# Performance work log

Measured on AMD Instinct MI355X. Metric: run time of the kernel, lower is better.

The kernel has to match this reference:

```python
import jax, jax.numpy as jnp
import numpy as np

B, SEQ, EMB, HID = 256, 256, 128, 512
NG = 1          # n_glimpses
CEXP = 10.0     # tanh_exploration
NEG = -1e9      # masked-logit value (stands in for -inf)


def setup_inputs():
    key = jax.random.key(0)
    ks = jax.random.split(key, 19)
    se = 1.0 / np.sqrt(EMB)
    sh = 1.0 / np.sqrt(HID)
    u = lambda k, shape, s: jax.random.uniform(k, shape, jnp.float32, -s, s)
    return {
        'embedding': u(ks[0], (SEQ, EMB), 1.0),
        'enc_Wih': u(ks[1], (4 * HID, EMB), sh),
        'enc_Whh': u(ks[2], (4 * HID, HID), sh),
        'enc_b': u(ks[3], (4 * HID,), sh),
        'dec_Wih': u(ks[4], (4 * HID, EMB), sh),
        'dec_Whh': u(ks[5], (4 * HID, HID), sh),
        'dec_b': u(ks[6], (4 * HID,), sh),
        'pt_Wq': u(ks[7], (HID, HID), sh), 'pt_bq': u(ks[8], (HID,), sh),
        'pt_Wref': u(ks[9], (HID, HID), sh), 'pt_bref': u(ks[10], (HID,), sh),
        'pt_V': u(ks[11], (HID,), sh),
        'gl_Wq': u(ks[12], (HID, HID), sh), 'gl_bq': u(ks[13], (HID,), sh),
        'gl_Wref': u(ks[14], (HID, HID), sh), 'gl_bref': u(ks[15], (HID,), sh),
        'gl_V': u(ks[16], (HID,), sh),
        'dec_start': u(ks[17], (EMB,), se),
        'inputs': jax.random.randint(ks[18], (B, SEQ), 0, SEQ),
    }


def lstm_cell(x, h, c, Wih, Whh, b):
    # PyTorch gate order: i, f, g, o
    g = x @ Wih.T + h @ Whh.T + b
    i, f, gg, o = jnp.split(g, 4, axis=1)
    c = jax.nn.sigmoid(f) * c + jax.nn.sigmoid(i) * jnp.tanh(gg)
    h = jax.nn.sigmoid(o) * jnp.tanh(c)
    return h, c


def reference(embedding, enc_Wih, enc_Whh, enc_b,
              dec_Wih, dec_Whh, dec_b,
              pt_Wq, pt_bq, pt_Wref, pt_bref, pt_V,
              gl_Wq, gl_bq, gl_Wref, gl_bref, gl_V,
              dec_start, inputs):
    emb = embedding[inputs]                      # [B,S,E]
    h0 = jnp.zeros((B, HID), jnp.float32)
    c0 = jnp.zeros((B, HID), jnp.float32)

    def enc_step(carry, x_t):
        h, c = carry
        h, c = lstm_cell(x_t, h, c, enc_Wih, enc_Whh, enc_b)
        return (h, c), h

    (h, c), hs = jax.lax.scan(enc_step, (h0, c0), jnp.swapaxes(emb, 0, 1))
    enc_out = jnp.swapaxes(hs, 0, 1)             # [B,S,H]

    # W_ref is a 1x1 Conv1d == per-position linear; precompute once (constant across steps)
    gl_ref = enc_out @ gl_Wref.T + gl_bref       # [B,S,H]
    pt_ref = enc_out @ pt_Wref.T + pt_bref       # [B,S,H]

    keys = jax.random.split(jax.random.key(1), SEQ)
    mask0 = jnp.zeros((B, SEQ), bool)
    dec_in0 = jnp.broadcast_to(dec_start, (B, EMB))

    def dec_step(carry, key_i):
        h, c, mask, dec_in = carry
        h, c = lstm_cell(dec_in, h, c, dec_Wih, dec_Whh, dec_b)
        q = h                                    # [B,H]
        for _ in range(NG):
            gl = jnp.tanh((q @ gl_Wq.T + gl_bq)[:, None, :] + gl_ref) @ gl_V  # [B,S]
            gl = jnp.where(mask, NEG, gl)
            q = jnp.einsum('bsh,bs->bh', gl_ref, jax.nn.softmax(gl, axis=1))
        lg = jnp.tanh((q @ pt_Wq.T + pt_bq)[:, None, :] + pt_ref) @ pt_V      # [B,S]
        lg = CEXP * jnp.tanh(lg)                 # use_tanh=True pointer
        lg = jnp.where(mask, NEG, lg)
        # Categorical sample via Gumbel-max
        gum = -jnp.log(-jnp.log(jax.random.uniform(key_i, (B, SEQ)) + 1e-10) + 1e-10)
        ptr = jnp.argmax(lg + gum, axis=1)       # [B]
        logp = jnp.take_along_axis(jax.nn.log_softmax(lg, axis=1), ptr[:, None], axis=1)[:, 0]
        mask = mask.at[jnp.arange(B), ptr].set(True)
        dec_in = emb[jnp.arange(B), ptr]         # embedding of chosen city
        return (h, c, mask, dec_in), (ptr, logp)

    _, (tours, logps) = jax.lax.scan(dec_step, (h, c, mask0, dec_in0), keys)
    return jnp.swapaxes(tours, 0, 1), jnp.swapaxes(logps, 0, 1)  # [B,S] each
```

## Files before the change

### kernel.cpp

```cpp
#include <hip/hip_runtime.h>
#include <math.h>


#define Bz 256
#define Sz 256
#define Ez 128
#define Hz 512
#define NEGV -1e9f
#define BH (Bz*Hz)

__device__ float g_encout[Bz*Sz*Hz];
__device__ float g_glref[Bz*Sz*Hz];
__device__ float g_ptref[Bz*Sz*Hz];
__device__ float g_h[2*BH];
__device__ float g_c[BH];
__device__ int g_ptrbuf[Bz];
__device__ unsigned g_keys[2*Sz];
__device__ unsigned char g_mask[Bz*Sz];

__device__ __forceinline__ unsigned rotl32(unsigned v, int d){ return (v<<d)|(v>>(32-d)); }

__device__ __forceinline__ void tf2x32(unsigned k0, unsigned k1, unsigned x0, unsigned x1,
                                       unsigned &o0, unsigned &o1){
  unsigned ks2 = k0 ^ k1 ^ 0x1BD11BDAu;
  x0 += k0; x1 += k1;
#define TFR(r) { x0 += x1; x1 = rotl32(x1,(r)); x1 ^= x0; }
  TFR(13) TFR(15) TFR(26) TFR(6)
  x0 += k1; x1 += ks2 + 1u;
  TFR(17) TFR(29) TFR(16) TFR(24)
  x0 += ks2; x1 += k0 + 2u;
  TFR(13) TFR(15) TFR(26) TFR(6)
  x0 += k0; x1 += k1 + 3u;
  TFR(17) TFR(29) TFR(16) TFR(24)
  x0 += k1; x1 += ks2 + 4u;
  TFR(13) TFR(15) TFR(26) TFR(6)
  x0 += ks2; x1 += k0 + 5u;
#undef TFR
  o0 = x0; o1 = x1;
}

__device__ __forceinline__ unsigned rng_bits(unsigned ka, unsigned kb, unsigned idx){
  unsigned o0,o1; tf2x32(ka,kb, 0u, idx, o0,o1);
  return o0 ^ o1;
}

__global__ __launch_bounds__(256) void init_kernel(){
  int i = blockIdx.x*256 + threadIdx.x;
  if (i < BH){ g_h[i] = 0.f; g_c[i] = 0.f; }
  if (i < Bz*Sz) g_mask[i] = 0;
  if (i < Sz){
    unsigned o0,o1; tf2x32(0u,1u, 0u, (unsigned)i, o0,o1);
    g_keys[2*i] = o0; g_keys[2*i+1] = o1;
  }
}

__global__ __launch_bounds__(256) void lstm_step(
    const float* __restrict__ Wih,
    const float* __restrict__ Whh,
    const float* __restrict__ bias,
    const float* __restrict__ emb_table,
    const int*   __restrict__ inputs,
    const float* __restrict__ dec_start,
    int t, int is_dec, int hsel)
{
  __shared__ float A_lds[64][36];
  __shared__ float W_lds[64][36];

  const float* h_in = g_h + (size_t)hsel*BH;
  float*       h_out = g_h + (size_t)(hsel^1)*BH;

  int tid = threadIdx.x;
  int bt = blockIdx.x;
  int jt = blockIdx.y;
  int jj = tid & 15;
  int bp = tid >> 4;
  int jglob = jt*16 + jj;
  int bq = bp*4;

  float acc[4][4];
  {
    float b0v = bias[jglob];
    float b1v = bias[Hz + jglob];
    float b2v = bias[2*Hz + jglob];
    float b3v = bias[3*Hz + jglob];
    #pragma unroll
    for (int r=0;r<4;r++){ acc[r][0]=b0v; acc[r][1]=b1v; acc[r][2]=b2v; acc[r][3]=b3v; }
  }

  int sr = tid >> 2;
  int sk = (tid & 3) * 8;
  int bg = bt*64 + sr;
  int wrow_g = (sr >> 4)*Hz + jt*16 + (sr & 15);

  for (int kc = 0; kc < 20; kc++){
    int k0 = kc*32;
    __syncthreads();
    {
      const float* src;
      if (k0 < Ez){
        const float* xrow;
        if (is_dec){
          xrow = (t == 0) ? dec_start
               : emb_table + (size_t)inputs[bg*Sz + g_ptrbuf[bg]] * Ez;
        } else {
          xrow = emb_table + (size_t)inputs[bg*Sz + t] * Ez;
        }
        src = xrow + k0 + sk;
      } else {
        src = h_in + (size_t)bg*Hz + (k0 - Ez) + sk;
      }
      float4 a0 = *(const float4*)src;
      float4 a1 = *(const float4*)(src + 4);
      *(float4*)&A_lds[sr][sk]     = a0;
      *(float4*)&A_lds[sr][sk + 4] = a1;
    }
    {
      const float* wr = (k0 < Ez) ? (Wih + (size_t)wrow_g*Ez + k0 + sk)
                                  : (Whh + (size_t)wrow_g*Hz + (k0 - Ez) + sk);
      float4 w0 = *(const float4*)wr;
      float4 w1 = *(const float4*)(wr + 4);
      *(float4*)&W_lds[sr][sk]     = w0;
      *(float4*)&W_lds[sr][sk + 4] = w1;
    }
    __syncthreads();
    #pragma unroll
    for (int k4 = 0; k4 < 8; k4++){
      float4 w0 = *(const float4*)&W_lds[jj      ][k4*4];
      float4 w1 = *(const float4*)&W_lds[16 + jj ][k4*4];
      float4 w2 = *(const float4*)&W_lds[32 + jj ][k4*4];
      float4 w3 = *(const float4*)&W_lds[48 + jj ][k4*4];
      float4 a0 = *(const float4*)&A_lds[bq + 0][k4*4];
      float4 a1 = *(const float4*)&A_lds[bq + 1][k4*4];
      float4 a2 = *(const float4*)&A_lds[bq + 2][k4*4];
      float4 a3 = *(const float4*)&A_lds[bq + 3][k4*4];
#define LSTEP(c) \
      acc[0][0]=fmaf(a0.c,w0.c,acc[0][0]); acc[0][1]=fmaf(a0.c,w1.c,acc[0][1]); \
      acc[0][2]=fmaf(a0.c,w2.c,acc[0][2]); acc[0][3]=fmaf(a0.c,w3.c,acc[0][3]); \
      acc[1][0]=fmaf(a1.c,w0.c,acc[1][0]); acc[1][1]=fmaf(a1.c,w1.c,acc[1][1]); \
      acc[1][2]=fmaf(a1.c,w2.c,acc[1][2]); acc[1][3]=fmaf(a1.c,w3.c,acc[1][3]); \
      acc[2][0]=fmaf(a2.c,w0.c,acc[2][0]); acc[2][1]=fmaf(a2.c,w1.c,acc[2][1]); \
      acc[2][2]=fmaf(a2.c,w2.c,acc[2][2]); acc[2][3]=fmaf(a2.c,w3.c,acc[2][3]); \
      acc[3][0]=fmaf(a3.c,w0.c,acc[3][0]); acc[3][1]=fmaf(a3.c,w1.c,acc[3][1]); \
      acc[3][2]=fmaf(a3.c,w2.c,acc[3][2]); acc[3][3]=fmaf(a3.c,w3.c,acc[3][3]);
      LSTEP(x) LSTEP(y) LSTEP(z) LSTEP(w)
#undef LSTEP
    }
  }

  #pragma unroll
  for (int r=0;r<4;r++){
    int b = bt*64 + bq + r;
    float gi = acc[r][0], gf = acc[r][1], gg = acc[r][2], go = acc[r][3];
    float co = g_c[(size_t)b*Hz + jglob];
    float si = 1.f/(1.f + expf(-gi));
    float sf = 1.f/(1.f + expf(-gf));
    float so = 1.f/(1.f + expf(-go));
    float cn = sf*co + si*tanhf(gg);
    float hn = so*tanhf(cn);
    g_c[(size_t)b*Hz + jglob] = cn;
    h_out[(size_t)b*Hz + jglob] = hn;
    if (!is_dec) g_encout[((size_t)b*Sz + t)*Hz + jglob] = hn;
  }
}

__global__ __launch_bounds__(256) void gemm_ref(
    const float* __restrict__ W, const float* __restrict__ bias, int dst_id)
{
  const float* A = g_encout;
  float*       C = (dst_id == 1) ? g_glref : g_ptref;
  __shared__ float As[32][68];
  __shared__ float Ws[32][68];
  int tid = threadIdx.x;
  int mt = blockIdx.x * 64, nt = blockIdx.y * 64;
  int tm = (tid & 15) * 4, tn = (tid >> 4) * 4;
  float acc[4][4] = {};
  int lr = tid >> 2;
  int lk = (tid & 3) * 8;

  for (int kc = 0; kc < 16; kc++){
    int k0 = kc*32;
    __syncthreads();
    {
      const float* ar = A + (size_t)(mt + lr)*Hz + k0 + lk;
      float4 a0 = *(const float4*)ar, a1 = *(const float4*)(ar+4);
      As[lk+0][lr]=a0.x; As[lk+1][lr]=a0.y; As[lk+2][lr]=a0.z; As[lk+3][lr]=a0.w;
      As[lk+4][lr]=a1.x; As[lk+5][lr]=a1.y; As[lk+6][lr]=a1.z; As[lk+7][lr]=a1.w;
      const float* wr = W + (size_t)(nt + lr)*Hz + k0 + lk;
      float4 w0 = *(const float4*)wr, w1 = *(const float4*)(wr+4);
      Ws[lk+0][lr]=w0.x; Ws[lk+1][lr]=w0.y; Ws[lk+2][lr]=w0.z; Ws[lk+3][lr]=w0.w;
      Ws[lk+4][lr]=w1.x; Ws[lk+5][lr]=w1.y; Ws[lk+6][lr]=w1.z; Ws[lk+7][lr]=w1.w;
    }
    __syncthreads();
    #pragma unroll
    for (int k=0;k<32;k++){
      float4 av = *(const float4*)&As[k][tm];
      float4 wv = *(const float4*)&Ws[k][tn];
      acc[0][0]=fmaf(av.x,wv.x,acc[0][0]); acc[0][1]=fmaf(av.x,wv.y,acc[0][1]);
      acc[0][2]=fmaf(av.x,wv.z,acc[0][2]); acc[0][3]=fmaf(av.x,wv.w,acc[0][3]);
      acc[1][0]=fmaf(av.y,wv.x,acc[1][0]); acc[1][1]=fmaf(av.y,wv.y,acc[1][1]);
      acc[1][2]=fmaf(av.y,wv.z,acc[1][2]); acc[1][3]=fmaf(av.y,wv.w,acc[1][3]);
      acc[2][0]=fmaf(av.z,wv.x,acc[2][0]); acc[2][1]=fmaf(av.z,wv.y,acc[2][1]);
      acc[2][2]=fmaf(av.z,wv.z,acc[2][2]); acc[2][3]=fmaf(av.z,wv.w,acc[2][3]);
      acc[3][0]=fmaf(av.w,wv.x,acc[3][0]); acc[3][1]=fmaf(av.w,wv.y,acc[3][1]);
      acc[3][2]=fmaf(av.w,wv.z,acc[3][2]); acc[3][3]=fmaf(av.w,wv.w,acc[3][3]);
    }
  }
  float b0v = bias[nt+tn+0], b1v = bias[nt+tn+1], b2v = bias[nt+tn+2], b3v = bias[nt+tn+3];
  #pragma unroll
  for (int i=0;i<4;i++){
    float4 o;
    o.x = acc[i][0] + b0v; o.y = acc[i][1] + b1v;
    o.z = acc[i][2] + b2v; o.w = acc[i][3] + b3v;
    *(float4*)(C + (size_t)(mt + tm + i)*Hz + nt + tn) = o;
  }
}

__global__ __launch_bounds__(1024) void attn_step(
    const float* __restrict__ gl_Wq, const float* __restrict__ gl_bq,
    const float* __restrict__ gl_V,
    const float* __restrict__ pt_Wq, const float* __restrict__ pt_bq,
    const float* __restrict__ pt_V,
    int t, int hsel2, float* __restrict__ out)
{
  int b = blockIdx.x, tid = threadIdx.x;
  int wave = tid >> 6, lane64 = tid & 63;
  int g = tid >> 5, lane = tid & 31;

  __shared__ __align__(16) float hq[Hz];
  __shared__ __align__(16) float q2s[Hz];
  __shared__ __align__(16) float qgs[Hz];
  __shared__ __align__(16) float qps[Hz];
  __shared__ __align__(16) float vgl[Hz];
  __shared__ __align__(16) float vpt[Hz];
  __shared__ float part[32][513];
  __shared__ float m_arr[32];
  __shared__ float l_arr[32];
  __shared__ float slog[Sz];
  __shared__ float redy[16]; __shared__ int redi[16];
  __shared__ float redm[16]; __shared__ float redsum[16];

  if (tid < Hz){
    hq[tid]  = g_h[(size_t)hsel2*BH + (size_t)b*Hz + tid];
    vgl[tid] = gl_V[tid];
    vpt[tid] = pt_V[tid];
  }
  __syncthreads();

  const unsigned char* mrow = g_mask + b*Sz;

  {
    float hv[8];
    #pragma unroll
    for (int i=0;i<8;i++) hv[i] = hq[lane64*8 + i];
    for (int jj=0;jj<32;jj++){
      int j = wave*32 + jj;
      const float* wr = gl_Wq + (size_t)j*Hz + lane64*8;
      float4 w0 = *(const float4*)wr;
      float4 w1 = *(const float4*)(wr+4);
      float p = 0.f;
      p = fmaf(hv[0], w0.x, p); p = fmaf(hv[1], w0.y, p);
      p = fmaf(hv[2], w0.z, p); p = fmaf(hv[3], w0.w, p);
      p = fmaf(hv[4], w1.x, p); p = fmaf(hv[5], w1.y, p);
      p = fmaf(hv[6], w1.z, p); p = fmaf(hv[7], w1.w, p);
      #pragma unroll
      for (int off=32; off; off>>=1) p += __shfl_xor(p, off);
      if (lane64 == 0) q2s[j] = p + gl_bq[j];
    }
  }
  __syncthreads();

  const float* glbase = g_glref + (size_t)b*Sz*Hz;
  {
    float m_g = -INFINITY, l_g = 0.f;
    float4 racc[4];
    { float4 z = {0.f,0.f,0.f,0.f}; racc[0]=z; racc[1]=z; racc[2]=z; racc[3]=z; }

    for (int r = 0; r < 8; r++){
      int s = g*8 + r;
      if (mrow[s]) continue;
      const float4* row4 = (const float4*)(glbase + (size_t)s*Hz);
      float4 x0 = row4[lane], x1 = row4[lane+32], x2 = row4[lane+64], x3 = row4[lane+96];
      float p = 0.f;
      {
        float4 q, vv;
        q = *(const float4*)&q2s[lane*4];        vv = *(const float4*)&vgl[lane*4];
        p = fmaf(vv.x, tanhf(q.x + x0.x), p); p = fmaf(vv.y, tanhf(q.y + x0.y), p);
        p = fmaf(vv.z, tanhf(q.z + x0.z), p); p = fmaf(vv.w, tanhf(q.w + x0.w), p);
        q = *(const float4*)&q2s[(lane+32)*4];   vv = *(const float4*)&vgl[(lane+32)*4];
        p = fmaf(vv.x, tanhf(q.x + x1.x), p); p = fmaf(vv.y, tanhf(q.y + x1.y), p);
        p = fmaf(vv.z, tanhf(q.z + x1.z), p); p = fmaf(vv.w, tanhf(q.w + x1.w), p);
        q = *(const float4*)&q2s[(lane+64)*4];   vv = *(const float4*)&vgl[(lane+64)*4];
        p = fmaf(vv.x, tanhf(q.x + x2.x), p); p = fmaf(vv.y, tanhf(q.y + x2.y), p);
        p = fmaf(vv.z, tanhf(q.z + x2.z), p); p = fmaf(vv.w, tanhf(q.w + x2.w), p);
        q = *(const float4*)&q2s[(lane+96)*4];   vv = *(const float4*)&vgl[(lane+96)*4];
        p = fmaf(vv.x, tanhf(q.x + x3.x), p); p = fmaf(vv.y, tanhf(q.y + x3.y), p);
        p = fmaf(vv.z, tanhf(q.z + x3.z), p); p = fmaf(vv.w, tanhf(q.w + x3.w), p);
      }
      #pragma unroll
      for (int off=16; off; off>>=1) p += __shfl_xor(p, off, 32);
      float lgv = p;
      if (lgv > m_g){
        float r_ = expf(m_g - lgv);
        l_g *= r_;
        racc[0].x*=r_; racc[0].y*=r_; racc[0].z*=r_; racc[0].w*=r_;
        racc[1].x*=r_; racc[1].y*=r_; racc[1].z*=r_; racc[1].w*=r_;
        racc[2].x*=r_; racc[2].y*=r_; racc[2].z*=r_; racc[2].w*=r_;
        racc[3].x*=r_; racc[3].y*=r_; racc[3].z*=r_; racc[3].w*=r_;
        m_g = lgv;
      }
      float pr = expf(lgv - m_g);
      l_g += pr;
      racc[0].x=fmaf(pr,x0.x,racc[0].x); racc[0].y=fmaf(pr,x0.y,racc[0].y);
      racc[0].z=fmaf(pr,x0.z,racc[0].z); racc[0].w=fmaf(pr,x0.w,racc[0].w);
      racc[1].x=fmaf(pr,x1.x,racc[1].x); racc[1].y=fmaf(pr,x1.y,racc[1].y);
      racc[1].z=fmaf(pr,x1.z,racc[1].z); racc[1].w=fmaf(pr,x1.w,racc[1].w);
      racc[2].x=fmaf(pr,x2.x,racc[2].x); racc[2].y=fmaf(pr,x2.y,racc[2].y);
      racc[2].z=fmaf(pr,x2.z,racc[2].z); racc[2].w=fmaf(pr,x2.w,racc[2].w);
      racc[3].x=fmaf(pr,x3.x,racc[3].x); racc[3].y=fmaf(pr,x3.y,racc[3].y);
      racc[3].z=fmaf(pr,x3.z,racc[3].z); racc[3].w=fmaf(pr,x3.w,racc[3].w);
    }
    if (lane == 0){ m_arr[g] = m_g; l_arr[g] = l_g; }
    part[g][4*lane+  0] = racc[0].x; part[g][4*lane+  1] = racc[0].y;
    part[g][4*lane+  2] = racc[0].z; part[g][4*lane+  3] = racc[0].w;
    part[g][4*lane+128] = racc[1].x; part[g][4*lane+129] = racc[1].y;
    part[g][4*lane+130] = racc[1].z; part[g][4*lane+131] = racc[1].w;
    part[g][4*lane+256] = racc[2].x; part[g][4*lane+257] = racc[2].y;
    part[g][4*lane+258] = racc[2].z; part[g][4*lane+259] = racc[2].w;
    part[g][4*lane+384] = racc[3].x; part[g][4*lane+385] = racc[3].y;
    part[g][4*lane+386] = racc[3].z; part[g][4*lane+387] = racc[3].w;
  }
  __syncthreads();

  if (tid < Hz){
    float M = m_arr[0];
    #pragma unroll
    for (int gg=1; gg<32; gg++) M = fmaxf(M, m_arr[gg]);
    float num = 0.f, den = 0.f;
    #pragma unroll
    for (int gg=0; gg<32; gg++){
      float w = expf(m_arr[gg] - M);
      num = fmaf(w, part[gg][tid], num);
      den = fmaf(w, l_arr[gg], den);
    }
    qgs[tid] = num / den;
  }
  __syncthreads();

  {
    float qv[8];
    #pragma unroll
    for (int i=0;i<8;i++) qv[i] = qgs[lane64*8 + i];
    for (int jj=0;jj<32;jj++){
      int j = wave*32 + jj;
      const float* wr = pt_Wq + (size_t)j*Hz + lane64*8;
      float4 w0 = *(const float4*)wr;
      float4 w1 = *(const float4*)(wr+4);
      float p = 0.f;
      p = fmaf(qv[0], w0.x, p); p = fmaf(qv[1], w0.y, p);
      p = fmaf(qv[2], w0.z, p); p = fmaf(qv[3], w0.w, p);
      p = fmaf(qv[4], w1.x, p); p = fmaf(qv[5], w1.y, p);
      p = fmaf(qv[6], w1.z, p); p = fmaf(qv[7], w1.w, p);
      #pragma unroll
      for (int off=32; off; off>>=1) p += __shfl_xor(p, off);
      if (lane64 == 0) qps[j] = p + pt_bq[j];
    }
  }
  __syncthreads();

  const float* ptbase = g_ptref + (size_t)b*Sz*Hz;
  for (int r = 0; r < 8; r++){
    int s = g*8 + r;
    float lgv;
    if (mrow[s]) lgv = NEGV;
    else {
      const float4* row4 = (const float4*)(ptbase + (size_t)s*Hz);
      float p = 0.f;
      #pragma unroll
      for (int i=0;i<4;i++){
        int idx = lane + i*32;
        float4 x  = row4[idx];
        float4 q  = *(const float4*)&qps[idx*4];
        float4 vv = *(const float4*)&vpt[idx*4];
        p = fmaf(vv.x, tanhf(q.x + x.x), p);
        p = fmaf(vv.y, tanhf(q.y + x.y), p);
        p = fmaf(vv.z, tanhf(q.z + x.z), p);
        p = fmaf(vv.w, tanhf(q.w + x.w), p);
      }
      #pragma unroll
      for (int off=16; off; off>>=1) p += __shfl_xor(p, off, 32);
      lgv = 10.f * tanhf(p);
    }
    if (lane == 0) slog[s] = lgv;
  }
  __syncthreads();

  float lg = NEGV, y = -INFINITY;
  if (tid < Sz){
    lg = slog[tid];
    unsigned bits = rng_bits(g_keys[2*t], g_keys[2*t+1], (unsigned)(b*Sz + tid));
    float u = __uint_as_float((bits >> 9) | 0x3f800000u) - 1.f;
    float gum = -logf(-logf(u + 1e-10f) + 1e-10f);
    y = lg + gum;
  }
  float by = y; int bi = tid; float bm = lg;
  #pragma unroll
  for (int off=32; off; off>>=1){
    float oy = __shfl_xor(by, off);
    int   oi = __shfl_xor(bi, off);
    float om = __shfl_xor(bm, off);
    if (oy > by || (oy == by && oi < bi)){ by = oy; bi = oi; }
    bm = fmaxf(bm, om);
  }
  if (lane64 == 0){ redy[wave] = by; redi[wave] = bi; redm[wave] = bm; }
  __syncthreads();
  float fy = redy[0]; int fi = redi[0]; float fm = redm[0];
  #pragma unroll
  for (int w=1; w<16; w++){
    if (redy[w] > fy || (redy[w] == fy && redi[w] < fi)){ fy = redy[w]; fi = redi[w]; }
    fm = fmaxf(fm, redm[w]);
  }
  int ptr = fi;

  float pe = (tid < Sz) ? expf(lg - fm) : 0.f;
  #pragma unroll
  for (int off=32; off; off>>=1) pe += __shfl_xor(pe, off);
  if (lane64 == 0) redsum[wave] = pe;
  __syncthreads();
  if (tid == 0){
    float den = 0.f;
    #pragma unroll
    for (int w=0; w<16; w++) den += redsum[w];
    float logp = slog[ptr] - fm - logf(den);
    out[(size_t)b*Sz + t] = (float)ptr;
    out[(size_t)Bz*Sz + (size_t)b*Sz + t] = logp;
    g_mask[b*Sz + ptr] = 1;
    g_ptrbuf[b] = ptr;
  }
}

extern "C" void kernel_launch(void* const* d_in, const int* in_sizes, int n_in,
                              void* d_out, int out_size, void* d_ws, size_t ws_size,
                              hipStream_t stream){
  (void)in_sizes; (void)n_in; (void)out_size; (void)d_ws; (void)ws_size;
  const float* embedding = (const float*)d_in[0];
  const float* enc_Wih = (const float*)d_in[1];
  const float* enc_Whh = (const float*)d_in[2];
  const float* enc_b   = (const float*)d_in[3];
  const float* dec_Wih = (const float*)d_in[4];
  const float* dec_Whh = (const float*)d_in[5];
  const float* dec_b   = (const float*)d_in[6];
  const float* pt_Wq   = (const float*)d_in[7];
  const float* pt_bq   = (const float*)d_in[8];
  const float* pt_Wref = (const float*)d_in[9];
  const float* pt_bref = (const float*)d_in[10];
  const float* pt_V    = (const float*)d_in[11];
  const float* gl_Wq   = (const float*)d_in[12];
  const float* gl_bq   = (const float*)d_in[13];
  const float* gl_Wref = (const float*)d_in[14];
  const float* gl_bref = (const float*)d_in[15];
  const float* gl_V    = (const float*)d_in[16];
  const float* dec_start = (const float*)d_in[17];
  const int*   inputs  = (const int*)d_in[18];
  float* out = (float*)d_out;

  init_kernel<<<512, 256, 0, stream>>>();

  for (int t = 0; t < Sz; t++){
    lstm_step<<<dim3(4,32), 256, 0, stream>>>(enc_Wih, enc_Whh, enc_b,
        embedding, inputs, dec_start, t, 0, t & 1);
  }
  gemm_ref<<<dim3(1024,8), 256, 0, stream>>>(gl_Wref, gl_bref, 1);
  gemm_ref<<<dim3(1024,8), 256, 0, stream>>>(pt_Wref, pt_bref, 2);

  for (int t = 0; t < Sz; t++){
    lstm_step<<<dim3(4,32), 256, 0, stream>>>(dec_Wih, dec_Whh, dec_b,
        embedding, inputs, dec_start, t, 1, t & 1);
    attn_step<<<Bz, 1024, 0, stream>>>(gl_Wq, gl_bq, gl_V,
        pt_Wq, pt_bq, pt_V, t, (t+1) & 1, out);
  }
}
```

Baseline: 43.45 ms.

## Precompute input projections per city, retile LSTM, compact unmasked rows in attention

Adds a kernel that precomputes Wih·x+b for all 256 embedding rows plus the decoder start token, so each LSTM step only runs the 512-wide Whh GEMM and gathers the input projection by city index. The LSTM step is retiled to 32 batch rows per block, giving twice as many blocks. The attention kernel drops from 1024 to 512 threads, builds a per-group list of unmasked positions with a ballot so glimpse and pointer loops visit only live rows with software prefetch, and processes two Wq rows per iteration. The trade-offs are extra global tables, lower per-block thread parallelism, and more uneven work across groups as the mask fills.

Result: faster. 34.79 ms (-19.9%).

```diff
diff --git a/kernel.cpp b/kernel.cpp
--- a/kernel.cpp
+++ b/kernel.cpp
@@ -12,6 +12,8 @@
 __device__ float g_encout[Bz*Sz*Hz];
 __device__ float g_glref[Bz*Sz*Hz];
 __device__ float g_ptref[Bz*Sz*Hz];
+__device__ float g_xpe[256*2048];
+__device__ float g_xpd[257*2048];
 __device__ float g_h[2*BH];
 __device__ float g_c[BH];
 __device__ int g_ptrbuf[Bz];
@@ -54,20 +56,36 @@
   }
 }
 
+__global__ __launch_bounds__(256) void xproj_kernel(
+    const float* __restrict__ Wih, const float* __restrict__ bias,
+    const float* __restrict__ emb, const float* __restrict__ dstart,
+    int dst)
+{
+  float* Xp = dst ? g_xpd : g_xpe;
+  int c = blockIdx.x;
+  int row = blockIdx.y*256 + threadIdx.x;
+  __shared__ float xs[Ez];
+  if (threadIdx.x < Ez) xs[threadIdx.x] = (c < 256) ? emb[c*Ez + threadIdx.x]
+                                                    : dstart[threadIdx.x];
+  __syncthreads();
+  float a = bias[row];
+  const float* w = Wih + (size_t)row*Ez;
+  #pragma unroll 8
+  for (int k = 0; k < Ez; k++) a = fmaf(xs[k], w[k], a);
+  Xp[(size_t)c*2048 + row] = a;
+}
+
 __global__ __launch_bounds__(256) void lstm_step(
-    const float* __restrict__ Wih,
     const float* __restrict__ Whh,
-    const float* __restrict__ bias,
-    const float* __restrict__ emb_table,
     const int*   __restrict__ inputs,
-    const float* __restrict__ dec_start,
     int t, int is_dec, int hsel)
 {
-  __shared__ float A_lds[64][36];
+  __shared__ float A_lds[32][36];
   __shared__ float W_lds[64][36];
 
   const float* h_in = g_h + (size_t)hsel*BH;
   float*       h_out = g_h + (size_t)(hsel^1)*BH;
+  const float* Xp = is_dec ? g_xpd : g_xpe;
 
   int tid = threadIdx.x;
   int bt = blockIdx.x;
@@ -75,52 +93,47 @@
   int jj = tid & 15;
   int bp = tid >> 4;
   int jglob = jt*16 + jj;
-  int bq = bp*4;
-
-  float acc[4][4];
-  {
-    float b0v = bias[jglob];
-    float b1v = bias[Hz + jglob];
-    float b2v = bias[2*Hz + jglob];
-    float b3v = bias[3*Hz + jglob];
-    #pragma unroll
-    for (int r=0;r<4;r++){ acc[r][0]=b0v; acc[r][1]=b1v; acc[r][2]=b2v; acc[r][3]=b3v; }
-  }
-
-  int sr = tid >> 2;
-  int sk = (tid & 3) * 8;
-  int bg = bt*64 + sr;
-  int wrow_g = (sr >> 4)*Hz + jt*16 + (sr & 15);
-
-  for (int kc = 0; kc < 20; kc++){
+
+  int bA = bt*32 + bp*2, bB = bA + 1;
+  int cA, cB;
+  if (is_dec){
+    if (t == 0){ cA = 256; cB = 256; }
+    else { cA = inputs[bA*Sz + g_ptrbuf[bA]]; cB = inputs[bB*Sz + g_ptrbuf[bB]]; }
+  } else {
+    cA = inputs[bA*Sz + t]; cB = inputs[bB*Sz + t];
+  }
+
+  float acc[2][4];
+  {
+    const float* xa = Xp + (size_t)cA*2048;
+    const float* xb = Xp + (size_t)cB*2048;
+    #pragma unroll
+    for (int g=0; g<4; g++){
+      acc[0][g] = xa[g*Hz + jglob];
+      acc[1][g] = xb[g*Hz + jglob];
+    }
+  }
+
+  int sr = tid >> 3;
+  int sk = (tid & 7) * 4;
+  int wr = tid >> 2;
+  int wk = (tid & 3) * 8;
+  int bg = bt*32 + sr;
+  int wrow_g = (wr >> 4)*Hz + jt*16 + (wr & 15);
+
+  for (int kc = 0; kc < 16; kc++){
     int k0 = kc*32;
     __syncthreads();
     {
-      const float* src;
-      if (k0 < Ez){
-        const float* xrow;
-        if (is_dec){
-          xrow = (t == 0) ? dec_start
-               : emb_table + (size_t)inputs[bg*Sz + g_ptrbuf[bg]] * Ez;
-        } else {
-          xrow = emb_table + (size_t)inputs[bg*Sz + t] * Ez;
-        }
-        src = xrow + k0 + sk;
-      } else {
-        src = h_in + (size_t)bg*Hz + (k0 - Ez) + sk;
-      }
-      float4 a0 = *(const float4*)src;
-      float4 a1 = *(const float4*)(src + 4);
-      *(float4*)&A_lds[sr][sk]     = a0;
-      *(float4*)&A_lds[sr][sk + 4] = a1;
+      float4 av = *(const float4*)(h_in + (size_t)bg*Hz + k0 + sk);
+      *(float4*)&A_lds[sr][sk] = av;
     }
     {
-      const float* wr = (k0 < Ez) ? (Wih + (size_t)wrow_g*Ez + k0 + sk)
-                                  : (Whh + (size_t)wrow_g*Hz + (k0 - Ez) + sk);
-      float4 w0 = *(const float4*)wr;
-      float4 w1 = *(const float4*)(wr + 4);
-      *(float4*)&W_lds[sr][sk]     = w0;
-      *(float4*)&W_lds[sr][sk + 4] = w1;
+      const float* ws = Whh + (size_t)wrow_g*Hz + k0 + wk;
+      float4 w0 = *(const float4*)ws;
+      float4 w1 = *(const float4*)(ws + 4);
+      *(float4*)&W_lds[wr][wk]     = w0;
+      *(float4*)&W_lds[wr][wk + 4] = w1;
     }
     __syncthreads();
     #pragma unroll
@@ -129,27 +142,21 @@
       float4 w1 = *(const float4*)&W_lds[16 + jj ][k4*4];
       float4 w2 = *(const float4*)&W_lds[32 + jj ][k4*4];
       float4 w3 = *(const float4*)&W_lds[48 + jj ][k4*4];
-      float4 a0 = *(const float4*)&A_lds[bq + 0][k4*4];
-      float4 a1 = *(const float4*)&A_lds[bq + 1][k4*4];
-      float4 a2 = *(const float4*)&A_lds[bq + 2][k4*4];
-      float4 a3 = *(const float4*)&A_lds[bq + 3][k4*4];
+      float4 a0 = *(const float4*)&A_lds[bp*2    ][k4*4];
+      float4 a1 = *(const float4*)&A_lds[bp*2 + 1][k4*4];
 #define LSTEP(c) \
       acc[0][0]=fmaf(a0.c,w0.c,acc[0][0]); acc[0][1]=fmaf(a0.c,w1.c,acc[0][1]); \
       acc[0][2]=fmaf(a0.c,w2.c,acc[0][2]); acc[0][3]=fmaf(a0.c,w3.c,acc[0][3]); \
       acc[1][0]=fmaf(a1.c,w0.c,acc[1][0]); acc[1][1]=fmaf(a1.c,w1.c,acc[1][1]); \
-      acc[1][2]=fmaf(a1.c,w2.c,acc[1][2]); acc[1][3]=fmaf(a1.c,w3.c,acc[1][3]); \
-      acc[2][0]=fmaf(a2.c,w0.c,acc[2][0]); acc[2][1]=fmaf(a2.c,w1.c,acc[2][1]); \
-      acc[2][2]=fmaf(a2.c,w2.c,acc[2][2]); acc[2][3]=fmaf(a2.c,w3.c,acc[2][3]); \
-      acc[3][0]=fmaf(a3.c,w0.c,acc[3][0]); acc[3][1]=fmaf(a3.c,w1.c,acc[3][1]); \
-      acc[3][2]=fmaf(a3.c,w2.c,acc[3][2]); acc[3][3]=fmaf(a3.c,w3.c,acc[3][3]);
+      acc[1][2]=fmaf(a1.c,w2.c,acc[1][2]); acc[1][3]=fmaf(a1.c,w3.c,acc[1][3]);
       LSTEP(x) LSTEP(y) LSTEP(z) LSTEP(w)
 #undef LSTEP
     }
   }
 
   #pragma unroll
-  for (int r=0;r<4;r++){
-    int b = bt*64 + bq + r;
+  for (int r=0;r<2;r++){
+    int b = bA + r;
     float gi = acc[r][0], gf = acc[r][1], gg = acc[r][2], go = acc[r][3];
     float co = g_c[(size_t)b*Hz + jglob];
     float si = 1.f/(1.f + expf(-gi));
@@ -185,8 +192,8 @@
       float4 a0 = *(const float4*)ar, a1 = *(const float4*)(ar+4);
       As[lk+0][lr]=a0.x; As[lk+1][lr]=a0.y; As[lk+2][lr]=a0.z; As[lk+3][lr]=a0.w;
       As[lk+4][lr]=a1.x; As[lk+5][lr]=a1.y; As[lk+6][lr]=a1.z; As[lk+7][lr]=a1.w;
-      const float* wr = W + (size_t)(nt + lr)*Hz + k0 + lk;
-      float4 w0 = *(const float4*)wr, w1 = *(const float4*)(wr+4);
+      const float* wrp = W + (size_t)(nt + lr)*Hz + k0 + lk;
+      float4 w0 = *(const float4*)wrp, w1 = *(const float4*)(wrp+4);
       Ws[lk+0][lr]=w0.x; Ws[lk+1][lr]=w0.y; Ws[lk+2][lr]=w0.z; Ws[lk+3][lr]=w0.w;
       Ws[lk+4][lr]=w1.x; Ws[lk+5][lr]=w1.y; Ws[lk+6][lr]=w1.z; Ws[lk+7][lr]=w1.w;
     }
@@ -215,7 +222,7 @@
   }
 }
 
-__global__ __launch_bounds__(1024) void attn_step(
+__global__ __launch_bounds__(512) void attn_step(
     const float* __restrict__ gl_Wq, const float* __restrict__ gl_bq,
     const float* __restrict__ gl_V,
     const float* __restrict__ pt_Wq, const float* __restrict__ pt_bq,
@@ -232,39 +239,61 @@
   __shared__ __align__(16) float qps[Hz];
   __shared__ __align__(16) float vgl[Hz];
   __shared__ __align__(16) float vpt[Hz];
-  __shared__ float part[32][513];
-  __shared__ float m_arr[32];
-  __shared__ float l_arr[32];
+  __shared__ float part[16][513];
+  __shared__ float m_arr[16];
+  __shared__ float l_arr[16];
+  __shared__ int   rlist[16][16];
   __shared__ float slog[Sz];
-  __shared__ float redy[16]; __shared__ int redi[16];
-  __shared__ float redm[16]; __shared__ float redsum[16];
-
-  if (tid < Hz){
-    hq[tid]  = g_h[(size_t)hsel2*BH + (size_t)b*Hz + tid];
-    vgl[tid] = gl_V[tid];
-    vpt[tid] = pt_V[tid];
-  }
+  __shared__ float redy[8]; __shared__ int redi[8];
+  __shared__ float redm[8]; __shared__ float redsum[8];
+
+  hq[tid]  = g_h[(size_t)hsel2*BH + (size_t)b*Hz + tid];
+  vgl[tid] = gl_V[tid];
+  vpt[tid] = pt_V[tid];
   __syncthreads();
 
   const unsigned char* mrow = g_mask + b*Sz;
 
+  int cnt;
+  {
+    bool un = (lane < 16) ? (mrow[g*16 + lane] == 0) : false;
+    unsigned long long bal = __ballot(un);
+    unsigned m16 = (unsigned)((g & 1) ? (bal >> 32) : bal) & 0xFFFFu;
+    cnt = __popc(m16);
+    if (lane < 16){
+      if (un){
+        int rank = __popc(m16 & ((1u << lane) - 1u));
+        rlist[g][rank] = g*16 + lane;
+      } else {
+        slog[g*16 + lane] = NEGV;
+      }
+    }
+  }
+
   {
     float hv[8];
     #pragma unroll
     for (int i=0;i<8;i++) hv[i] = hq[lane64*8 + i];
-    for (int jj=0;jj<32;jj++){
-      int j = wave*32 + jj;
-      const float* wr = gl_Wq + (size_t)j*Hz + lane64*8;
-      float4 w0 = *(const float4*)wr;
-      float4 w1 = *(const float4*)(wr+4);
-      float p = 0.f;
-      p = fmaf(hv[0], w0.x, p); p = fmaf(hv[1], w0.y, p);
-      p = fmaf(hv[2], w0.z, p); p = fmaf(hv[3], w0.w, p);
-      p = fmaf(hv[4], w1.x, p); p = fmaf(hv[5], w1.y, p);
-      p = fmaf(hv[6], w1.z, p); p = fmaf(hv[7], w1.w, p);
+    for (int jj=0;jj<64;jj+=2){
+      int j0 = wave*64 + jj;
+      const float* wr0 = gl_Wq + (size_t)j0*Hz + lane64*8;
+      const float* wr1 = wr0 + Hz;
+      float4 A0 = *(const float4*)wr0, A1 = *(const float4*)(wr0+4);
+      float4 B0 = *(const float4*)wr1, B1 = *(const float4*)(wr1+4);
+      float p0 = 0.f, p1 = 0.f;
+      p0 = fmaf(hv[0], A0.x, p0); p0 = fmaf(hv[1], A0.y, p0);
+      p0 = fmaf(hv[2], A0.z, p0); p0 = fmaf(hv[3], A0.w, p0);
+      p0 = fmaf(hv[4], A1.x, p0); p0 = fmaf(hv[5], A1.y, p0);
+      p0 = fmaf(hv[6], A1.z, p0); p0 = fmaf(hv[7], A1.w, p0);
+      p1 = fmaf(hv[0], B0.x, p1); p1 = fmaf(hv[1], B0.y, p1);
+      p1 = fmaf(hv[2], B0.z, p1); p1 = fmaf(hv[3], B0.w, p1);
+      p1 = fmaf(hv[4], B1.x, p1); p1 = fmaf(hv[5], B1.y, p1);
+      p1 = fmaf(hv[6], B1.z, p1); p1 = fmaf(hv[7], B1.w, p1);
       #pragma unroll
-      for (int off=32; off; off>>=1) p += __shfl_xor(p, off);
-      if (lane64 == 0) q2s[j] = p + gl_bq[j];
+      for (int off=32; off; off>>=1) p0 += __shfl_xor(p0, off);
+      #pragma unroll
+      for (int off=32; off; off>>=1) p1 += __shfl_xor(p1, off);
+      if (lane64 == 0){ q2s[j0] = p0 + gl_bq[j0]; q2s[j0+1] = p1 + gl_bq[j0+1]; }
     }
   }
   __syncthreads();
@@ -275,11 +304,17 @@
     float4 racc[4];
     { float4 z = {0.f,0.f,0.f,0.f}; racc[0]=z; racc[1]=z; racc[2]=z; racc[3]=z; }
 
-    for (int r = 0; r < 8; r++){
-      int s = g*8 + r;
-      if (mrow[s]) continue;
-      const float4* row4 = (const float4*)(glbase + (size_t)s*Hz);
-      float4 x0 = row4[lane], x1 = row4[lane+32], x2 = row4[lane+64], x3 = row4[lane+96];
+    float4 xn0, xn1, xn2, xn3;
+    if (cnt > 0){
+      const float4* rp = (const float4*)(glbase + (size_t)rlist[g][0]*Hz);
+      xn0 = rp[lane]; xn1 = rp[lane+32]; xn2 = rp[lane+64]; xn3 = rp[lane+96];
+    }
+    for (int i = 0; i < cnt; i++){
+      float4 x0 = xn0, x1 = xn1, x2 = xn2, x3 = xn3;
+      if (i + 1 < cnt){
+        const float4* rp = (const float4*)(glbase + (size_t)rlist[g][i+1]*Hz);
+        xn0 = rp[lane]; xn1 = rp[lane+32]; xn2 = rp[lane+64]; xn3 = rp[lane+96];
+      }
       float p = 0.f;
       {
         float4 q, vv;
@@ -331,13 +366,13 @@
   }
   __syncthreads();
 
-  if (tid < Hz){
+  {
     float M = m_arr[0];
     #pragma unroll
-    for (int gg=1; gg<32; gg++) M = fmaxf(M, m_arr[gg]);
+    for (int gg=1; gg<16; gg++) M = fmaxf(M, m_arr[gg]);
     float num = 0.f, den = 0.f;
     #pragma unroll
-    for (int gg=0; gg<32; gg++){
+    for (int gg=0; gg<16; gg++){
       float w = expf(m_arr[gg] - M);
       num = fmaf(w, part[gg][tid], num);
       den = fmaf(w, l_arr[gg], den);
@@ -350,47 +385,64 @@
     float qv[8];
     #pragma unroll
     for (int i=0;i<8;i++) qv[i] = qgs[lane64*8 + i];
-    for (int jj=0;jj<32;jj++){
-      int j = wave*32 + jj;
-      const float* wr = pt_Wq + (size_t)j*Hz + lane64*8;
-      float4 w0 = *(const float4*)wr;
-      float4 w1 = *(const float4*)(wr+4);
+    for (int jj=0;jj<64;jj+=2){
+      int j0 = wave*64 + jj;
+      const float* wr0 = pt_Wq + (size_t)j0*Hz + lane64*8;
+      const float* wr1 = wr0 + Hz;
+      float4 A0 = *(const float4*)wr0, A1 = *(const float4*)(wr0+4);
+      float4 B0 = *(const float4*)wr1, B1 = *(const float4*)(wr1+4);
+      float p0 = 0.f, p1 = 0.f;
+      p0 = fmaf(qv[0], A0.x, p0); p0 = fmaf(qv[1], A0.y, p0);
+      p0 = fmaf(qv[2], A0.z, p0); p0 = fmaf(qv[3], A0.w, p0);
+      p0 = fmaf(qv[4], A1.x, p0); p0 = fmaf(qv[5], A1.y, p0);
+      p0 = fmaf(qv[6], A1.z, p0); p0 = fmaf(qv[7], A1.w, p0);
+      p1 = fmaf(qv[0], B0.x, p1); p1 = fmaf(qv[1], B0.y, p1);
+      p1 = fmaf(qv[2], B0.z, p1); p1 = fmaf(qv[3], B0.w, p1);
+      p1 = fmaf(qv[4], B1.x, p1); p1 = fmaf(qv[5], B1.y, p1);
+      p1 = fmaf(qv[6], B1.z, p1); p1 = fmaf(qv[7], B1.w, p1);
+      #pragma unroll
+      for (int off=32; off; off>>=1) p0 += __shfl_xor(p0, off);
+      #pragma unroll
+      for (int off=32; off; off>>=1) p1 += __shfl_xor(p1, off);
+      if (lane64 == 0){ qps[j0] = p0 + pt_bq[j0]; qps[j0+1] = p1 + pt_bq[j0+1]; }
+    }
+  }
+  __syncthreads();
+
+  const float* ptbase = g_ptref + (size_t)b*Sz*Hz;
+  {
+    float4 xn0, xn1, xn2, xn3;
+    if (cnt > 0){
+      const float4* rp = (const float4*)(ptbase + (size_t)rlist[g][0]*Hz);
+      xn0 = rp[lane]; xn1 = rp[lane+32]; xn2 = rp[lane+64]; xn3 = rp[lane+96];
+    }
+    for (int i = 0; i < cnt; i++){
+      int s = rlist[g][i];
+      float4 x0 = xn0, x1 = xn1, x2 = xn2, x3 = xn3;
+      if (i + 1 < cnt){
+        const float4* rp = (const float4*)(ptbase + (size_t)rlist[g][i+1]*Hz);
+        xn0 = rp[lane]; xn1 = rp[lane+32]; xn2 = rp[lane+64]; xn3 = rp[lane+96];
+      }
       float p = 0.f;
-      p = fmaf(qv[0], w0.x, p); p = fmaf(qv[1], w0.y, p);
-      p = fmaf(qv[2], w0.z, p); p = fmaf(qv[3], w0.w, p);
-      p = fmaf(qv[4], w1.x, p); p = fmaf(qv[5], w1.y, p);
-      p = fmaf(qv[6], w1.z, p); p = fmaf(qv[7], w1.w, p);
-      #pragma unroll
-      for (int off=32; off; off>>=1) p += __shfl_xor(p, off);
-      if (lane64 == 0) qps[j] = p + pt_bq[j];
-    }
-  }
-  __syncthreads();
-
-  const float* ptbase = g_ptref + (size_t)b*Sz*Hz;
-  for (int r = 0; r < 8; r++){
-    int s = g*8 + r;
-    float lgv;
-    if (mrow[s]) lgv = NEGV;
-    else {
-      const float4* row4 = (const float4*)(ptbase + (size_t)s*Hz);
-      float p = 0.f;
-      #pragma unroll
-      for (int i=0;i<4;i++){
-        int idx = lane + i*32;
-        float4 x  = row4[idx];
-        float4 q  = *(const float4*)&qps[idx*4];
-        float4 vv = *(const float4*)&vpt[idx*4];
-        p = fmaf(vv.x, tanhf(q.x + x.x), p);
-        p = fmaf(vv.y, tanhf(q.y + x.y), p);
-        p = fmaf(vv.z, tanhf(q.z + x.z), p);
-        p = fmaf(vv.w, tanhf(q.w + x.w), p);
+      {
+        float4 q, vv;
+        q = *(const float4*)&qps[lane*4];        vv = *(const float4*)&vpt[lane*4];
+        p = fmaf(vv.x, tanhf(q.x + x0.x), p); p = fmaf(vv.y, tanhf(q.y + x0.y), p);
+        p = fmaf(vv.z, tanhf(q.z + x0.z), p); p = fmaf(vv.w, tanhf(q.w + x0.w), p);
+        q = *(const float4*)&qps[(lane+32)*4];   vv = *(const float4*)&vpt[(lane+32)*4];
+        p = fmaf(vv.x, tanhf(q.x + x1.x), p); p = fmaf(vv.y, tanhf(q.y + x1.y), p);
+        p = fmaf(vv.z, tanhf(q.z + x1.z), p); p = fmaf(vv.w, tanhf(q.w + x1.w), p);
+        q = *(const float4*)&qps[(lane+64)*4];   vv = *(const float4*)&vpt[(lane+64)*4];
+        p = fmaf(vv.x, tanhf(q.x + x2.x), p); p = fmaf(vv.y, tanhf(q.y + x2.y), p);
+        p = fmaf(vv.z, tanhf(q.z + x2.z), p); p = fmaf(vv.w, tanhf(q.w + x2.w), p);
+        q = *(const float4*)&qps[(lane+96)*4];   vv = *(const float4*)&vpt[(lane+96)*4];
+        p = fmaf(vv.x, tanhf(q.x + x3.x), p); p = fmaf(vv.y, tanhf(q.y + x3.y), p);
+        p = fmaf(vv.z, tanhf(q.z + x3.z), p); p = fmaf(vv.w, tanhf(q.w + x3.w), p);
       }
       #pragma unroll
       for (int off=16; off; off>>=1) p += __shfl_xor(p, off, 32);
-      lgv = 10.f * tanhf(p);
-    }
-    if (lane == 0) slog[s] = lgv;
+      if (lane == 0) slog[s] = 10.f * tanhf(p);
+    }
   }
   __syncthreads();
 
@@ -415,7 +467,7 @@
   __syncthreads();
   float fy = redy[0]; int fi = redi[0]; float fm = redm[0];
   #pragma unroll
-  for (int w=1; w<16; w++){
+  for (int w=1; w<8; w++){
     if (redy[w] > fy || (redy[w] == fy && redi[w] < fi)){ fy = redy[w]; fi = redi[w]; }
     fm = fmaxf(fm, redm[w]);
   }
@@ -427,9 +479,8 @@
   if (lane64 == 0) redsum[wave] = pe;
   __syncthreads();
   if (tid == 0){
-    float den = 0.f;
-    #pragma unroll
-    for (int w=0; w<16; w++) den += redsum[w];
+    float den = ((redsum[0]+redsum[1]) + (redsum[2]+redsum[3]))
+              + ((redsum[4]+redsum[5]) + (redsum[6]+redsum[7]));
     float logp = slog[ptr] - fm - logf(den);
     out[(size_t)b*Sz + t] = (float)ptr;
     out[(size_t)Bz*Sz + (size_t)b*Sz + t] = logp;
@@ -464,18 +515,18 @@
   float* out = (float*)d_out;
 
   init_kernel<<<512, 256, 0, stream>>>();
+  xproj_kernel<<<dim3(256,8), 256, 0, stream>>>(enc_Wih, enc_b, embedding, dec_start, 0);
+  xproj_kernel<<<dim3(257,8), 256, 0, stream>>>(dec_Wih, dec_b, embedding, dec_start, 1);
 
   for (int t = 0; t < Sz; t++){
-    lstm_step<<<dim3(4,32), 256, 0, stream>>>(enc_Wih, enc_Whh, enc_b,
-        embedding, inputs, dec_start, t, 0, t & 1);
+    lstm_step<<<dim3(8,32), 256, 0, stream>>>(enc_Whh, inputs, t, 0, t & 1);
   }
   gemm_ref<<<dim3(1024,8), 256, 0, stream>>>(gl_Wref, gl_bref, 1);
   gemm_ref<<<dim3(1024,8), 256, 0, stream>>>(pt_Wref, pt_bref, 2);
 
   for (int t = 0; t < Sz; t++){
-    lstm_step<<<dim3(4,32), 256, 0, stream>>>(dec_Wih, dec_Whh, dec_b,
-        embedding, inputs, dec_start, t, 1, t & 1);
-    attn_step<<<Bz, 1024, 0, stream>>>(gl_Wq, gl_bq, gl_V,
+    lstm_step<<<dim3(8,32), 256, 0, stream>>>(dec_Whh, inputs, t, 1, t & 1);
+    attn_step<<<Bz, 512, 0, stream>>>(gl_Wq, gl_bq, gl_V,
         pt_Wq, pt_bq, pt_V, t, (t+1) & 1, out);
   }
 }
```
